# Performance work log

Measured on AMD Instinct MI355X. Metric: run time of the kernel, lower is better.

Reference implementation:

```python
import jax, jax.numpy as jnp
import numpy as np

ALPHA = 0.5
WIN_SIZE = 31
BN_EPS = 1e-5
LRELU_SLOPE = 0.1


def setup_inputs() -> dict:
    key = jax.random.key(0)
    k1, k2, k3, k4 = jax.random.split(key, 4)
    B, N, C, P, E = 4, 2048, 64, 48, 128
    return {
        "sig_new": jax.random.normal(k1, (B, N, C, P), dtype=jnp.float32),
        "atten_mem": jax.random.normal(k2, (B, N, C, P), dtype=jnp.float32),
        "conv_w": jax.random.normal(k3, (E, C, P), dtype=jnp.float32) * 0.05,
        "conv_b": jax.random.normal(k4, (E,), dtype=jnp.float32) * 0.05,
        "bn_gamma": jnp.ones((E,), dtype=jnp.float32),
        "bn_beta": jnp.zeros((E,), dtype=jnp.float32),
    }


def _neighbour_mask(n_cutout):
    # clamped banded mask (pano_scan=False / training-mode branch)
    half = WIN_SIZE // 2
    cols = jnp.clip(jnp.arange(n_cutout)[:, None] + jnp.arange(-half, half + 1)[None, :], 0, n_cutout - 1)
    rows = jnp.broadcast_to(jnp.arange(n_cutout)[:, None], cols.shape)
    return jnp.zeros((n_cutout, n_cutout), jnp.float32).at[rows, cols].set(1.0)


def _embed(x, conv_w, conv_b, bn_gamma, bn_beta, B, N):
    # Conv1d(kernel=n_pts) on length-n_pts input == full contraction over (c, p)
    y = jnp.einsum("ncp,ecp->ne", x.reshape(-1, x.shape[-2], x.shape[-1]), conv_w) + conv_b
    # BatchNorm1d, training-mode batch statistics over the (B*N) batch dim
    mu = y.mean(axis=0)
    var = ((y - mu) ** 2).mean(axis=0)
    y = (y - mu) * jax.lax.rsqrt(var + BN_EPS) * bn_gamma + bn_beta
    y = jnp.where(y >= 0, y, LRELU_SLOPE * y)  # LeakyReLU(0.1)
    return y.reshape(B, N, -1)


def reference(sig_new, atten_mem, conv_w, conv_b, bn_gamma, bn_beta):
    B, N, C, P = sig_new.shape
    mask = _neighbour_mask(N)
    embed_x = _embed(sig_new, conv_w, conv_b, bn_gamma, bn_beta, B, N)      # [B,N,E]
    embed_t = _embed(atten_mem, conv_w, conv_b, bn_gamma, bn_beta, B, N)    # [B,N,E]
    sim = jnp.einsum("bie,bje->bij", embed_x, embed_t)                      # [B,N,N]
    sim = sim - 1e10 * (1.0 - mask)
    mx = jnp.max(sim, axis=-1, keepdims=True)
    ex = jnp.exp(sim - mx) * mask
    attn = ex / jnp.sum(ex, axis=-1, keepdims=True)                          # [B,N,N]
    mem_flat = atten_mem.reshape(B, N, C * P)
    mem_w = jnp.einsum("bij,bjf->bif", attn, mem_flat).reshape(B, N, C, P)
    new_mem = ALPHA * sig_new + (1.0 - ALPHA) * mem_w
    return new_mem, attn
```

## Files before the change

kernel.cpp:

```cpp
#include <hip/hip_runtime.h>

#define BATCH 4
#define NDIM 2048
#define EDIM 128
#define KDIM 3072
#define MDIM 8192
#define HALF 15

typedef __attribute__((ext_vector_type(8))) short short8v;
typedef __attribute__((ext_vector_type(4))) float f32x4;

__device__ inline ushort bf16h(float x) {
  union { float f; unsigned u; } v; v.f = x;
  unsigned r = v.u + 0x7fff + ((v.u >> 16) & 1);
  return (ushort)(r >> 16);
}

__global__ __launch_bounds__(256)
void k_wprep(const float* __restrict__ w, ushort* __restrict__ wh, ushort* __restrict__ wl) {
  const int q = (blockIdx.x * 256 + threadIdx.x) * 4;
  float4 v = *(const float4*)(w + q);
  const float f[4] = {v.x, v.y, v.z, v.w};
  ushort4 h, l;
  ushort* ph = (ushort*)&h; ushort* pl = (ushort*)&l;
#pragma unroll
  for (int j = 0; j < 4; ++j) {
    unsigned u = __float_as_uint(f[j]);
    ph[j] = (ushort)(u >> 16);
    pl[j] = bf16h(f[j] - __uint_as_float(u & 0xffff0000u));
  }
  *(ushort4*)(wh + q) = h;
  *(ushort4*)(wl + q) = l;
}

#define BMT 128
#define BK 64
#define SWZ(row, k) (((row) << 6) + (((((k) >> 3) ^ ((row) & 7)) << 3) | ((k) & 7)))

__global__ __launch_bounds__(256, 2)
void k_gemm(const float* __restrict__ x0, const float* __restrict__ x1,
            const ushort* __restrict__ wh, const ushort* __restrict__ wl,
            float* __restrict__ part, int splitK) {
  const int tid = threadIdx.x;
  const int m0 = blockIdx.x * BMT;
  const int kc = blockIdx.y;
  const int inp = blockIdx.z;
  const float* __restrict__ x = inp ? x1 : x0;
  const int kpc = KDIM / splitK;
  const int kbeg = kc * kpc;
  const int nsteps = kpc / BK;

  __shared__ ushort sAh[BMT * BK];
  __shared__ ushort sAl[BMT * BK];
  __shared__ ushort sBh[EDIM * BK];
  __shared__ ushort sBl[EDIM * BK];

  const int srow = tid >> 2;
  const int skb = (tid & 3) << 4;

  const int lane = tid & 63;
  const int wid = tid >> 6;
  const int wr = wid >> 1;
  const int wc = wid & 1;
  const int fr = lane & 15;
  const int kg = (lane >> 4) << 3;

  f32x4 acc[4][4];
#pragma unroll
  for (int a = 0; a < 4; ++a)
#pragma unroll
    for (int b = 0; b < 4; ++b) acc[a][b] = (f32x4){0.f, 0.f, 0.f, 0.f};

  float4 rA[2][4];
  ushort4 rBh[2][4], rBl[2][4];
  {
    const float* xb = x + (size_t)(m0 + srow) * KDIM + kbeg + skb;
    const ushort* wb = wh + (size_t)srow * KDIM + kbeg + skb;
    const ushort* wb2 = wl + (size_t)srow * KDIM + kbeg + skb;
#pragma unroll
    for (int h = 0; h < 2; ++h)
#pragma unroll
      for (int j = 0; j < 4; ++j) {
        rA[h][j]  = *(const float4*)(xb + (size_t)(64 * h) * KDIM + 4 * j);
        rBh[h][j] = *(const ushort4*)(wb + (size_t)(64 * h) * KDIM + 4 * j);
        rBl[h][j] = *(const ushort4*)(wb2 + (size_t)(64 * h) * KDIM + 4 * j);
      }
  }

  for (int st = 0; st < nsteps; ++st) {
    __syncthreads();
#pragma unroll
    for (int h = 0; h < 2; ++h) {
      const int row = srow + 64 * h;
#pragma unroll
      for (int j = 0; j < 4; ++j) {
        const int k = skb + 4 * j;
        const float fa[4] = {rA[h][j].x, rA[h][j].y, rA[h][j].z, rA[h][j].w};
        ushort4 ah, al;
        ushort* pah = (ushort*)&ah; ushort* pal = (ushort*)&al;
#pragma unroll
        for (int t = 0; t < 4; ++t) {
          unsigned u = __float_as_uint(fa[t]);
          pah[t] = (ushort)(u >> 16);
          pal[t] = bf16h(fa[t] - __uint_as_float(u & 0xffff0000u));
        }
        *(ushort4*)&sAh[SWZ(row, k)] = ah;
        *(ushort4*)&sAl[SWZ(row, k)] = al;
        *(ushort4*)&sBh[SWZ(row, k)] = rBh[h][j];
        *(ushort4*)&sBl[SWZ(row, k)] = rBl[h][j];
      }
    }
    __syncthreads();

    if (st + 1 < nsteps) {
      const int ko = kbeg + (st + 1) * BK + skb;
      const float* xb = x + (size_t)(m0 + srow) * KDIM + ko;
      const ushort* wb = wh + (size_t)srow * KDIM + ko;
      const ushort* wb2 = wl + (size_t)srow * KDIM + ko;
#pragma unroll
      for (int h = 0; h < 2; ++h)
#pragma unroll
        for (int j = 0; j < 4; ++j) {
          rA[h][j]  = *(const float4*)(xb + (size_t)(64 * h) * KDIM + 4 * j);
          rBh[h][j] = *(const ushort4*)(wb + (size_t)(64 * h) * KDIM + 4 * j);
          rBl[h][j] = *(const ushort4*)(wb2 + (size_t)(64 * h) * KDIM + 4 * j);
        }
    }

#pragma unroll
    for (int kk = 0; kk < 2; ++kk) {
      const int kb2 = kg + 32 * kk;
      short8v ah[4], al[4], bh[4], bl[4];
#pragma unroll
      for (int mi = 0; mi < 4; ++mi) {
        const int row = wr * 64 + mi * 16 + fr;
        ah[mi] = *(const short8v*)&sAh[SWZ(row, kb2)];
        al[mi] = *(const short8v*)&sAl[SWZ(row, kb2)];
      }
#pragma unroll
      for (int ei = 0; ei < 4; ++ei) {
        const int e = wc * 64 + ei * 16 + fr;
        bh[ei] = *(const short8v*)&sBh[SWZ(e, kb2)];
        bl[ei] = *(const short8v*)&sBl[SWZ(e, kb2)];
      }
#pragma unroll
      for (int mi = 0; mi < 4; ++mi)
#pragma unroll
        for (int ei = 0; ei < 4; ++ei) {
          acc[mi][ei] = __builtin_amdgcn_mfma_f32_16x16x32_bf16(ah[mi], bh[ei], acc[mi][ei], 0, 0, 0);
          acc[mi][ei] = __builtin_amdgcn_mfma_f32_16x16x32_bf16(ah[mi], bl[ei], acc[mi][ei], 0, 0, 0);
          acc[mi][ei] = __builtin_amdgcn_mfma_f32_16x16x32_bf16(al[mi], bh[ei], acc[mi][ei], 0, 0, 0);
        }
    }
  }

  float* po = part + ((size_t)(inp * splitK + kc) * MDIM + m0) * EDIM;
#pragma unroll
  for (int mi = 0; mi < 4; ++mi) {
    const int mloc = wr * 64 + mi * 16 + ((lane >> 4) << 2);
#pragma unroll
    for (int ei = 0; ei < 4; ++ei) {
      const int e = wc * 64 + ei * 16 + fr;
#pragma unroll
      for (int r = 0; r < 4; ++r)
        po[(size_t)(mloc + r) * EDIM + e] = acc[mi][ei][r];
    }
  }
}

__global__ __launch_bounds__(256)
void k_reduce(const float* __restrict__ part, const float* __restrict__ bvec,
              float* __restrict__ y, float* __restrict__ spart, int splitK) {
  const int tid = threadIdx.x;
  const int in = blockIdx.z;
  const int rb = blockIdx.x;
  const int e = tid & 127;
  const int rh = tid >> 7;
  const float bb = bvec[e];
  float s = 0.f, s2 = 0.f;
  for (int rr = 0; rr < 32; ++rr) {
    const int r = rb * 64 + rh * 32 + rr;
    float v = 0.f;
    for (int kc = 0; kc < splitK; ++kc)
      v += part[((size_t)(in * splitK + kc) * MDIM + r) * EDIM + e];
    v += bb;
    y[((size_t)in * MDIM + r) * EDIM + e] = v;
    s += v; s2 += v * v;
  }
  __shared__ float l1[256], l2[256];
  l1[tid] = s; l2[tid] = s2;
  __syncthreads();
  if (rh == 0) {
    s = l1[e] + l1[e + 128];
    s2 = l2[e] + l2[e + 128];
    spart[((size_t)(in * 128 + rb) * 2 + 0) * 128 + e] = s;
    spart[((size_t)(in * 128 + rb) * 2 + 1) * 128 + e] = s2;
  }
}

__global__ void k_finalize(const float* __restrict__ spart, const float* __restrict__ gamma,
                           const float* __restrict__ beta, float* __restrict__ scsh) {
  const int in = blockIdx.x;
  const int e = threadIdx.x;
  float s = 0.f, s2 = 0.f;
  for (int rb = 0; rb < 128; ++rb) {
    s  += spart[((size_t)(in * 128 + rb) * 2 + 0) * 128 + e];
    s2 += spart[((size_t)(in * 128 + rb) * 2 + 1) * 128 + e];
  }
  const float mu = s * (1.f / MDIM);
  const float var = s2 * (1.f / MDIM) - mu * mu;
  const float rs = rsqrtf(var + 1e-5f);
  const float sc = gamma[e] * rs;
  const float sh = beta[e] - mu * sc;
  scsh[in * 128 + e] = sc;
  scsh[256 + in * 128 + e] = sh;
}

#define SIMW 34
#define SIMP 132

__global__ __launch_bounds__(256)
void k_sim(const float* __restrict__ y, const float* __restrict__ scsh,
           float* __restrict__ attn, float* __restrict__ aw) {
  const int tid = threadIdx.x;
  const int bid = blockIdx.x;
  const int b = bid >> 9;
  const int i0 = (bid << 2) & 2047;
  const int jlo = max(0, i0 - HALF);
  const int jhi = min(NDIM - 1, i0 + 3 + HALF);
  const int tw = jhi - jlo + 1;

  __shared__ float sT[SIMW][SIMP];
  __shared__ float sX[4][SIMP];
  __shared__ float sSc[2][128], sSh[2][128];

  if (tid < 128) { sSc[0][tid] = scsh[tid]; sSh[0][tid] = scsh[256 + tid]; }
  else { const int e = tid - 128; sSc[1][e] = scsh[128 + e]; sSh[1][e] = scsh[384 + e]; }
  __syncthreads();

  const int totq = (4 + tw) * 32;
  for (int q = tid; q < totq; q += 256) {
    const int rr = q >> 5;
    const int e4 = (q & 31) << 2;
    const bool isx = rr < 4;
    const int gr = isx ? ((b << 11) + i0 + rr)
                       : (MDIM + (b << 11) + jlo + (rr - 4));
    float4 v = *(const float4*)(y + (size_t)gr * EDIM + e4);
    const float* sc = isx ? sSc[0] : sSc[1];
    const float* sh = isx ? sSh[0] : sSh[1];
    const float* pv = (const float*)&v;
    float* dst = isx ? &sX[rr][e4] : &sT[rr - 4][e4];
#pragma unroll
    for (int t = 0; t < 4; ++t) {
      const float val = fmaf(sc[e4 + t], pv[t], sh[e4 + t]);
      dst[t] = val >= 0.f ? val : 0.1f * val;
    }
  }
  __syncthreads();

  const int lane = tid & 63;
  const int wv = tid >> 6;
  const int i = i0 + wv;
  const int row = (b << 11) + i;
  const int jliw = max(0, i - HALF);
  const int jhiw = min(NDIM - 1, i + HALF);
  const int j = jliw + lane;
  const bool valid = (lane < 31) && (j <= jhiw);
  const int trow = (valid ? j : jliw) - jlo;

  float s = 0.f;
#pragma unroll
  for (int e = 0; e < EDIM; e += 4) {
    float4 u = *(const float4*)&sX[wv][e];
    float4 v = *(const float4*)&sT[trow][e];
    s = fmaf(u.x, v.x, s); s = fmaf(u.y, v.y, s);
    s = fmaf(u.z, v.z, s); s = fmaf(u.w, v.w, s);
  }
  float sm = valid ? s : -1e30f;
  float mx = sm;
#pragma unroll
  for (int o = 1; o < 64; o <<= 1) mx = fmaxf(mx, __shfl_xor(mx, o));
  const float p = valid ? __expf(sm - mx) : 0.f;
  float ss = p;
#pragma unroll
  for (int o = 1; o < 64; o <<= 1) ss += __shfl_xor(ss, o);
  const float a = p / ss;

  float* orow = attn + (size_t)row * NDIM;
  const int bw = jhiw - jliw;
  for (int c0 = lane << 2; c0 < NDIM; c0 += 256) {
    float4 v;
    float* pv = (float*)&v;
#pragma unroll
    for (int t = 0; t < 4; ++t) {
      const int d = c0 + t - jliw;
      const float val = __shfl(a, d & 63);
      pv[t] = (d >= 0 && d <= bw) ? val : 0.f;
    }
    *(float4*)(orow + c0) = v;
  }
  if (lane < 32) aw[(size_t)row * 32 + lane] = valid ? a : 0.f;
}

#define TI 16
#define TJMAX 46
#define FCW 256
#define NWG2 (NDIM / TI * BATCH)

__global__ __launch_bounds__(256, 2)
void k_memw(const float* __restrict__ sig, const float* __restrict__ mem,
            const float* __restrict__ aw, float* __restrict__ out) {
  const int tid = threadIdx.x;
  const int bid = blockIdx.x;
  const int nid = (bid & 7) * (NWG2 / 8) + (bid >> 3);
  const int b = nid >> 7;
  const int i0 = (nid & 127) << 4;
  const int jlo = max(0, i0 - HALF);
  const int jhi = min(NDIM - 1, i0 + TI - 1 + HALF);
  const int tj = jhi - jlo + 1;

  __shared__ float sV[TJMAX][FCW];
  __shared__ float sWt[TJMAX][TI];

  for (int idx = tid; idx < tj * TI; idx += 256) {
    const int jj = idx >> 4;
    const int ii = idx & 15;
    const int ii_g = i0 + ii;
    const int jg = jlo + jj;
    const int jli = max(0, ii_g - HALF);
    const int jhii = min(NDIM - 1, ii_g + HALF);
    float wv = 0.f;
    if (jg >= jli && jg <= jhii) wv = aw[(size_t)((b << 11) + ii_g) * 32 + (jg - jli)];
    sWt[jj][ii] = wv;
  }

  const int ig = tid >> 6;
  const int fg = tid & 63;
  const int ibase = i0 + (ig << 2);
  const int wlo = max(jlo, ibase - HALF) - jlo;
  const int whi = min(jhi, ibase + 3 + HALF) - jlo;

  for (int fc0 = 0; fc0 < KDIM; fc0 += FCW) {
    for (int idx = tid; idx < tj * (FCW / 4); idx += 256) {
      const int jj = idx >> 6;
      const int f4 = idx & 63;
      *(float4*)&sV[jj][f4 << 2] =
          *(const float4*)(mem + (size_t)((b << 11) + jlo + jj) * KDIM + fc0 + (f4 << 2));
    }
    __syncthreads();

    float acc[4][4];
#pragma unroll
    for (int a = 0; a < 4; ++a)
#pragma unroll
      for (int c = 0; c < 4; ++c) acc[a][c] = 0.f;

    for (int jj = wlo; jj <= whi; ++jj) {
      float4 wv = *(const float4*)&sWt[jj][ig << 2];
      float4 vv = *(const float4*)&sV[jj][fg << 2];
      const float wa[4] = {wv.x, wv.y, wv.z, wv.w};
      const float va[4] = {vv.x, vv.y, vv.z, vv.w};
#pragma unroll
      for (int mi = 0; mi < 4; ++mi)
#pragma unroll
        for (int fi = 0; fi < 4; ++fi)
          acc[mi][fi] = fmaf(wa[mi], va[fi], acc[mi][fi]);
    }

    const size_t base = (size_t)((b << 11) + ibase) * KDIM + fc0 + (fg << 2);
#pragma unroll
    for (int mi = 0; mi < 4; ++mi) {
      float4 sv = *(const float4*)(sig + base + (size_t)mi * KDIM);
      float4 ov;
      ov.x = 0.5f * sv.x + 0.5f * acc[mi][0];
      ov.y = 0.5f * sv.y + 0.5f * acc[mi][1];
      ov.z = 0.5f * sv.z + 0.5f * acc[mi][2];
      ov.w = 0.5f * sv.w + 0.5f * acc[mi][3];
      *(float4*)(out + base + (size_t)mi * KDIM) = ov;
    }
    __syncthreads();
  }
}

extern "C" void kernel_launch(void* const* d_in, const int* in_sizes, int n_in,
                              void* d_out, int out_size, void* d_ws, size_t ws_size,
                              hipStream_t stream) {
  const float* sig   = (const float*)d_in[0];
  const float* mem   = (const float*)d_in[1];
  const float* w     = (const float*)d_in[2];
  const float* bv    = (const float*)d_in[3];
  const float* gamma = (const float*)d_in[4];
  const float* beta  = (const float*)d_in[5];

  float* out_mem  = (float*)d_out;
  float* out_attn = out_mem + (size_t)BATCH * NDIM * KDIM;

  float* wsf = (float*)d_ws;
  const size_t ME = (size_t)MDIM * EDIM;
  const size_t fixed = 2 * ME + 65536 + 512 + 262144 + 196608;
  int splitK = 4;
  while (splitK > 1 && ((size_t)2 * splitK * ME + fixed) * 4 > ws_size) splitK >>= 1;

  float* part  = wsf;
  float* y     = part + (size_t)2 * splitK * ME;
  float* spart = y + 2 * ME;
  float* scsh  = spart + 65536;
  float* aw    = scsh + 512;
  ushort* wh   = (ushort*)(aw + 262144);
  ushort* wl   = wh + (size_t)EDIM * KDIM;

  hipLaunchKernelGGL(k_wprep, dim3(EDIM * KDIM / 1024), dim3(256), 0, stream, w, wh, wl);

  dim3 g1(MDIM / BMT, splitK, 2);
  hipLaunchKernelGGL(k_gemm, g1, dim3(256), 0, stream, sig, mem, wh, wl, part, splitK);

  dim3 g2(MDIM / 64, 1, 2);
  hipLaunchKernelGGL(k_reduce, g2, dim3(256), 0, stream, part, bv, y, spart, splitK);

  hipLaunchKernelGGL(k_finalize, dim3(2), dim3(128), 0, stream, spart, gamma, beta, scsh);

  hipLaunchKernelGGL(k_sim, dim3(MDIM / 4), dim3(256), 0, stream, y, scsh, out_attn, aw);

  hipLaunchKernelGGL(k_memw, dim3(NWG2), dim3(256), 0, stream, sig, mem, aw, out_mem);
}
```

Baseline: 469.9 us.

## Register-prefetch next memory chunk and split feature dim across more workgroups

The weighted-memory kernel now prefetches the next 256-column slice of the memory rows into registers while computing on the current slice in shared memory, overlapping global loads with the FMA loop. The feature dimension is split in two halves across separate workgroups, doubling the grid, and launch bounds are raised to allow three blocks per CU. The cost is higher register pressure from 12 float4 prefetch registers under a tighter occupancy target, and the window rows of memory are loaded redundantly by twice as many blocks.

```diff
diff --git a/kernel.cpp b/kernel.cpp
--- a/kernel.cpp
+++ b/kernel.cpp
@@ -305,19 +305,25 @@
 #define TI 16
 #define TJMAX 46
 #define FCW 256
-#define NWG2 (NDIM / TI * BATCH)
-
-__global__ __launch_bounds__(256, 2)
+#define NFH 2
+#define CHUNKS (KDIM / FCW / NFH)
+#define NWG2 (NDIM / TI * BATCH * NFH)
+#define PREG 12
+
+__global__ __launch_bounds__(256, 3)
 void k_memw(const float* __restrict__ sig, const float* __restrict__ mem,
             const float* __restrict__ aw, float* __restrict__ out) {
   const int tid = threadIdx.x;
   const int bid = blockIdx.x;
   const int nid = (bid & 7) * (NWG2 / 8) + (bid >> 3);
-  const int b = nid >> 7;
+  const int fh = nid >> 9;
+  const int b = (nid >> 7) & 3;
   const int i0 = (nid & 127) << 4;
+  const int fcbase = fh * (KDIM / NFH);
   const int jlo = max(0, i0 - HALF);
   const int jhi = min(NDIM - 1, i0 + TI - 1 + HALF);
   const int tj = jhi - jlo + 1;
+  const int cnt = tj * (FCW / 4);
 
   __shared__ float sV[TJMAX][FCW];
   __shared__ float sWt[TJMAX][TI];
@@ -340,20 +346,41 @@
   const int wlo = max(jlo, ibase - HALF) - jlo;
   const int whi = min(jhi, ibase + 3 + HALF) - jlo;
 
-  for (int fc0 = 0; fc0 < KDIM; fc0 += FCW) {
-    for (int idx = tid; idx < tj * (FCW / 4); idx += 256) {
-      const int jj = idx >> 6;
-      const int f4 = idx & 63;
-      *(float4*)&sV[jj][f4 << 2] =
-          *(const float4*)(mem + (size_t)((b << 11) + jlo + jj) * KDIM + fc0 + (f4 << 2));
-    }
+  const float* __restrict__ memb = mem + (size_t)((b << 11) + jlo) * KDIM;
+
+  float4 cur[PREG];
+#pragma unroll
+  for (int t = 0; t < PREG; ++t) {
+    const int idx = tid + t * 256;
+    if (idx < cnt)
+      cur[t] = *(const float4*)(memb + (size_t)(idx >> 6) * KDIM + fcbase + ((idx & 63) << 2));
+  }
+
+  for (int c = 0; c < CHUNKS; ++c) {
+    const int fc0 = fcbase + c * FCW;
     __syncthreads();
+#pragma unroll
+    for (int t = 0; t < PREG; ++t) {
+      const int idx = tid + t * 256;
+      if (idx < cnt) *(float4*)&sV[idx >> 6][(idx & 63) << 2] = cur[t];
+    }
+    __syncthreads();
+
+    if (c + 1 < CHUNKS) {
+      const int fcn = fc0 + FCW;
+#pragma unroll
+      for (int t = 0; t < PREG; ++t) {
+        const int idx = tid + t * 256;
+        if (idx < cnt)
+          cur[t] = *(const float4*)(memb + (size_t)(idx >> 6) * KDIM + fcn + ((idx & 63) << 2));
+      }
+    }
 
     float acc[4][4];
 #pragma unroll
     for (int a = 0; a < 4; ++a)
 #pragma unroll
-      for (int c = 0; c < 4; ++c) acc[a][c] = 0.f;
+      for (int cc = 0; cc < 4; ++cc) acc[a][cc] = 0.f;
 
     for (int jj = wlo; jj <= whi; ++jj) {
       float4 wv = *(const float4*)&sWt[jj][ig << 2];
@@ -378,7 +405,6 @@
       ov.w = 0.5f * sv.w + 0.5f * acc[mi][3];
       *(float4*)(out + base + (size_t)mi * KDIM) = ov;
     }
-    __syncthreads();
   }
 }
 
```

Measured after the change: 572.2 us. 21.8% more time.
